# Kernel tuning notes

Measured on AMD Instinct MI355X. Metric: run time of the kernel, lower is better.

Reference implementation:

```python
import jax, jax.numpy as jnp
import numpy as np

B, L, C, NH = 4, 2048, 512, 8
HD = C // NH  # head_dim = 64


def setup_inputs() -> dict:
    key = jax.random.key(0)
    k1, k2, k3, k4 = jax.random.split(key, 4)
    s = 1.0 / np.sqrt(C)
    return {
        "x": jax.random.normal(k1, (B, L, C), dtype=jnp.float32),
        "w_qkv": jax.random.normal(k2, (C, 3 * C), dtype=jnp.float32) * s,
        "b_qkv": jnp.zeros((3 * C,), dtype=jnp.float32),  # zeroed in __init__
        "w_proj": jax.random.normal(k3, (C, C), dtype=jnp.float32) * s,
        "b_proj": jax.random.normal(k4, (C,), dtype=jnp.float32) * 0.01,
    }


def reference(x, w_qkv, b_qkv, w_proj, b_proj):
    Bx, Lx, Cx = x.shape
    qkv = x @ w_qkv + b_qkv                       # [B, L, 3C]
    qkv = qkv.reshape(Bx, Lx, 3, NH, HD)          # 'B L (K H D)'
    qkv = jnp.transpose(qkv, (2, 0, 3, 1, 4))     # 'K B H L D'
    q, k, v = qkv[0], qkv[1], qkv[2]
    scale = 1.0 / np.sqrt(HD)
    scores = jnp.einsum('bhld,bhmd->bhlm', q, k) * scale  # [B, H, L, L]
    attn = jax.nn.softmax(scores, axis=-1)
    out = jnp.einsum('bhlm,bhmd->bhld', attn, v)  # [B, H, L, D]
    out = jnp.transpose(out, (0, 2, 1, 3)).reshape(Bx, Lx, Cx)  # 'B H L D -> B L (H D)'
    return out @ w_proj + b_proj
```

## Files before the change

kernel.cpp:

```cpp
#include <hip/hip_runtime.h>
#include <math.h>

#define B_   4
#define L_   2048
#define C_   512
#define NH_  8
#define HD_  64
#define M_   (B_ * L_)
#define N_QKV 1536

typedef __bf16 bf16x8 __attribute__((ext_vector_type(8)));
typedef float floatx4 __attribute__((ext_vector_type(4)));

__device__ __forceinline__ unsigned pk_bf16(float a, float b) {
  union { float f; unsigned u; } x, y;
  x.f = a; y.f = b;
  unsigned lo = x.u + (0x7fffu + ((x.u >> 16) & 1u));
  unsigned hi = y.u + (0x7fffu + ((y.u >> 16) & 1u));
  return (lo >> 16) | (hi & 0xffff0000u);
}

__device__ __forceinline__ unsigned short bf16_1(float a) {
  union { float f; unsigned u; } x;
  x.f = a;
  return (unsigned short)((x.u + (0x7fffu + ((x.u >> 16) & 1u))) >> 16);
}

__device__ __forceinline__ floatx4 mfma16(bf16x8 a, bf16x8 b, floatx4 c) {
  return __builtin_amdgcn_mfma_f32_16x16x32_bf16(a, b, c, 0, 0, 0);
}

__device__ __forceinline__ void gld_lds16(const void* g, void* s) {
  __builtin_amdgcn_global_load_lds(
      (const __attribute__((address_space(1))) unsigned int*)(g),
      (__attribute__((address_space(3))) unsigned int*)(s), 16, 0, 0);
}

__global__ __launch_bounds__(256) void convert_x_kernel(
    const float* __restrict__ x, unsigned short* __restrict__ xb) {
  size_t i = ((size_t)blockIdx.x * 256 + threadIdx.x) * 8;
  float4 a = *(const float4*)(x + i);
  float4 b = *(const float4*)(x + i + 4);
  uint4 o;
  o.x = pk_bf16(a.x, a.y);
  o.y = pk_bf16(a.z, a.w);
  o.z = pk_bf16(b.x, b.y);
  o.w = pk_bf16(b.z, b.w);
  *(uint4*)(xb + i) = o;
}

__global__ __launch_bounds__(256) void convert_wt_kernel(
    const float* __restrict__ w, unsigned short* __restrict__ wt, int N) {
  __shared__ unsigned short tile[64][68];
  const int t = threadIdx.x;
  const int n0 = blockIdx.x * 64, k0 = blockIdx.y * 64;
  const int r = t >> 4, c4 = (t & 15) * 4;
#pragma unroll
  for (int i = 0; i < 4; ++i) {
    int k = r + i * 16;
    float4 v = *(const float4*)(w + (size_t)(k0 + k) * N + n0 + c4);
    uint2 p;
    p.x = pk_bf16(v.x, v.y);
    p.y = pk_bf16(v.z, v.w);
    *(uint2*)&tile[k][c4] = p;
  }
  __syncthreads();
#pragma unroll
  for (int i = 0; i < 4; ++i) {
    int n = r + i * 16;
    uint2 o;
    o.x = (unsigned)tile[c4 + 0][n] | ((unsigned)tile[c4 + 1][n] << 16);
    o.y = (unsigned)tile[c4 + 2][n] | ((unsigned)tile[c4 + 3][n] << 16);
    *(uint2*)(wt + (size_t)(n0 + n) * 512 + k0 + c4) = o;
  }
}

__global__ __launch_bounds__(256) void qkv_mfma_kernel(
    const unsigned short* __restrict__ A,
    const unsigned short* __restrict__ Bt,
    const float* __restrict__ bias,
    unsigned short* __restrict__ Qd, unsigned short* __restrict__ Kd,
    unsigned short* __restrict__ Vd) {
  __shared__ unsigned short As[4096];
  __shared__ unsigned short Bs[4096];

  const int t = threadIdx.x;
  const int w = t >> 6, l = t & 63;
  const int li = l & 15, lq = l >> 4;
  const int wm = w & 1, wn = w >> 1;
  const int m0 = blockIdx.x * 128;
  const int n0 = blockIdx.y * 128;

  const int inner = (l & 7) ^ (l >> 3);
  const int srow = (l >> 3) * 2 + (inner >> 2);
  const int skb = inner & 3;

  const unsigned short* asrc0 = A + (size_t)(m0 + (2 * w) * 16 + srow) * 512 + skb * 8;
  const unsigned short* asrc1 = A + (size_t)(m0 + (2 * w + 1) * 16 + srow) * 512 + skb * 8;
  const unsigned short* bsrc0 = Bt + (size_t)(n0 + (2 * w) * 16 + srow) * 512 + skb * 8;
  const unsigned short* bsrc1 = Bt + (size_t)(n0 + (2 * w + 1) * 16 + srow) * 512 + skb * 8;
  unsigned short* adst0 = &As[(2 * w) * 512];
  unsigned short* adst1 = &As[(2 * w + 1) * 512];
  unsigned short* bdst0 = &Bs[(2 * w) * 512];
  unsigned short* bdst1 = &Bs[(2 * w + 1) * 512];

  const int foff = (li >> 1) * 128 + ((((li & 1) * 4 + lq)) ^ (li >> 1)) * 16;

  const floatx4 fz = {0.f, 0.f, 0.f, 0.f};
  floatx4 acc[4][4];
#pragma unroll
  for (int i = 0; i < 4; ++i)
#pragma unroll
    for (int j = 0; j < 4; ++j) acc[i][j] = fz;

  for (int kk = 0; kk < 16; ++kk) {
    __syncthreads();
    gld_lds16(asrc0, adst0);
    gld_lds16(asrc1, adst1);
    gld_lds16(bsrc0, bdst0);
    gld_lds16(bsrc1, bdst1);
    asrc0 += 32; asrc1 += 32; bsrc0 += 32; bsrc1 += 32;
    __syncthreads();

    bf16x8 af[4], bf[4];
#pragma unroll
    for (int mt = 0; mt < 4; ++mt)
      af[mt] = *(const bf16x8*)((const char*)As + (wm * 64 + mt * 16) * 64 + foff);
#pragma unroll
    for (int nt = 0; nt < 4; ++nt)
      bf[nt] = *(const bf16x8*)((const char*)Bs + (wn * 64 + nt * 16) * 64 + foff);
#pragma unroll
    for (int mt = 0; mt < 4; ++mt)
#pragma unroll
      for (int nt = 0; nt < 4; ++nt)
        acc[mt][nt] = mfma16(af[mt], bf[nt], acc[mt][nt]);
  }

  const int n0g = n0 + wn * 64;
  const int kk2 = n0g >> 9, h = (n0g >> 6) & 7;
  const int mb = m0 + wm * 64;
  const int b = mb >> 11;
  float bb[4];
#pragma unroll
  for (int nt = 0; nt < 4; ++nt) bb[nt] = bias[n0g + nt * 16 + li];

  if (kk2 < 2) {
    unsigned short* outp = kk2 ? Kd : Qd;
#pragma unroll
    for (int mt = 0; mt < 4; ++mt) {
      int lrow = (mb + mt * 16 + lq * 4) & (L_ - 1);
#pragma unroll
      for (int nt = 0; nt < 4; ++nt) {
        int d = nt * 16 + li;
        unsigned short* p =
            outp + ((size_t)((b * NH_ + h) * L_ + lrow)) * HD_ + d;
#pragma unroll
        for (int r = 0; r < 4; ++r)
          p[(size_t)r * HD_] = bf16_1(acc[mt][nt][r] + bb[nt]);
      }
    }
  } else {
#pragma unroll
    for (int mt = 0; mt < 4; ++mt) {
      int lrow = (mb + mt * 16 + lq * 4) & (L_ - 1);
#pragma unroll
      for (int nt = 0; nt < 4; ++nt) {
        int d = nt * 16 + li;
        uint2 v;
        v.x = pk_bf16(acc[mt][nt][0] + bb[nt], acc[mt][nt][1] + bb[nt]);
        v.y = pk_bf16(acc[mt][nt][2] + bb[nt], acc[mt][nt][3] + bb[nt]);
        *(uint2*)(Vd + ((size_t)((b * NH_ + h) * HD_ + d)) * L_ + lrow) = v;
      }
    }
  }
}

__global__ __launch_bounds__(256) void proj_mfma_kernel(
    const unsigned short* __restrict__ A,
    const unsigned short* __restrict__ Bt,
    const float* __restrict__ bias, float* __restrict__ out) {
  __shared__ unsigned short As[2048];
  __shared__ unsigned short Bs[4096];

  const int t = threadIdx.x;
  const int w = t >> 6, l = t & 63;
  const int li = l & 15, lq = l >> 4;
  const int wm = w & 1, wn = w >> 1;
  const int m0 = blockIdx.x * 64;
  const int n0 = blockIdx.y * 128;

  const int inner = (l & 7) ^ (l >> 3);
  const int srow = (l >> 3) * 2 + (inner >> 2);
  const int skb = inner & 3;

  const unsigned short* asrc0 = A + (size_t)(m0 + w * 16 + srow) * 512 + skb * 8;
  const unsigned short* bsrc0 = Bt + (size_t)(n0 + (2 * w) * 16 + srow) * 512 + skb * 8;
  const unsigned short* bsrc1 = Bt + (size_t)(n0 + (2 * w + 1) * 16 + srow) * 512 + skb * 8;
  unsigned short* adst0 = &As[w * 512];
  unsigned short* bdst0 = &Bs[(2 * w) * 512];
  unsigned short* bdst1 = &Bs[(2 * w + 1) * 512];

  const int foff = (li >> 1) * 128 + ((((li & 1) * 4 + lq)) ^ (li >> 1)) * 16;

  const floatx4 fz = {0.f, 0.f, 0.f, 0.f};
  floatx4 acc[2][4];
#pragma unroll
  for (int i = 0; i < 2; ++i)
#pragma unroll
    for (int j = 0; j < 4; ++j) acc[i][j] = fz;

  for (int kk = 0; kk < 16; ++kk) {
    __syncthreads();
    gld_lds16(asrc0, adst0);
    gld_lds16(bsrc0, bdst0);
    gld_lds16(bsrc1, bdst1);
    asrc0 += 32; bsrc0 += 32; bsrc1 += 32;
    __syncthreads();

    bf16x8 af[2], bf[4];
#pragma unroll
    for (int mt = 0; mt < 2; ++mt)
      af[mt] = *(const bf16x8*)((const char*)As + (wm * 32 + mt * 16) * 64 + foff);
#pragma unroll
    for (int nt = 0; nt < 4; ++nt)
      bf[nt] = *(const bf16x8*)((const char*)Bs + (wn * 64 + nt * 16) * 64 + foff);
#pragma unroll
    for (int mt = 0; mt < 2; ++mt)
#pragma unroll
      for (int nt = 0; nt < 4; ++nt)
        acc[mt][nt] = mfma16(af[mt], bf[nt], acc[mt][nt]);
  }

#pragma unroll
  for (int mt = 0; mt < 2; ++mt) {
    int m = m0 + wm * 32 + mt * 16 + lq * 4;
#pragma unroll
    for (int nt = 0; nt < 4; ++nt) {
      int n = n0 + wn * 64 + nt * 16 + li;
      float bb = bias[n];
#pragma unroll
      for (int r = 0; r < 4; ++r)
        out[(size_t)(m + r) * C_ + n] = acc[mt][nt][r] + bb;
    }
  }
}

__global__ __launch_bounds__(256) void attn_kernel(
    const unsigned short* __restrict__ Qg, const unsigned short* __restrict__ Kg,
    const unsigned short* __restrict__ Vg, unsigned short* __restrict__ AO) {
  __shared__ unsigned short Ks[4096];
  __shared__ unsigned short Vt[4096];
  __shared__ unsigned short Ps[4][32][88];

  const int t  = threadIdx.x;
  const int w  = t >> 6;
  const int l  = t & 63;
  const int li = l & 15;
  const int lq = l >> 4;
  const int bh = blockIdx.y;
  const int m0 = blockIdx.x * 128;

  const unsigned short* ksrc[2];
  const unsigned short* vsrc[2];
  unsigned short* kdst[2];
  unsigned short* vdst[2];
#pragma unroll
  for (int u = 0; u < 2; ++u) {
    int q = 2 * w + u;
    int blk = q * 64 + l;
    int row = blk >> 3, sblk = blk & 7;
    int dblk = sblk ^ ((row >> 2) & 7);
    ksrc[u] = Kg + ((size_t)bh * L_ + row) * HD_ + dblk * 8;
    kdst[u] = &Ks[q * 512];
    int kblk = sblk ^ (row & 7);
    vsrc[u] = Vg + ((size_t)bh * HD_ + row) * L_ + kblk * 8;
    vdst[u] = &Vt[q * 512];
  }

  bf16x8 qf[2][2];
#pragma unroll
  for (int g = 0; g < 2; ++g)
#pragma unroll
    for (int s = 0; s < 2; ++s)
      qf[g][s] = *(const bf16x8*)(Qg +
          ((size_t)bh * L_ + m0 + w * 32 + 16 * g + li) * HD_ + s * 32 + lq * 8);

  const floatx4 fz = {0.f, 0.f, 0.f, 0.f};
  floatx4 O[2][4];
  float lsum[2][4];
#pragma unroll
  for (int g = 0; g < 2; ++g) {
#pragma unroll
    for (int dt = 0; dt < 4; ++dt) O[g][dt] = fz;
#pragma unroll
    for (int r = 0; r < 4; ++r) lsum[g][r] = 0.f;
  }

  const float SC = 0.18033688011f;

  for (int c = 0; c < L_ / 64; ++c) {
    __syncthreads();
#pragma unroll
    for (int u = 0; u < 2; ++u) {
      gld_lds16(ksrc[u], kdst[u]);
      gld_lds16(vsrc[u], vdst[u]);
      ksrc[u] += 64 * HD_;
      vsrc[u] += 64;
    }
    __syncthreads();

    floatx4 sa[2][4];
#pragma unroll
    for (int g = 0; g < 2; ++g)
#pragma unroll
      for (int kt = 0; kt < 4; ++kt) sa[g][kt] = fz;

#pragma unroll
    for (int s = 0; s < 2; ++s) {
#pragma unroll
      for (int kt = 0; kt < 4; ++kt) {
        int key = 4 * li + kt;
        int blk = key * 8 + ((lq + 4 * s) ^ (li & 7));
        bf16x8 kf = *(const bf16x8*)&Ks[blk * 8];
        sa[0][kt] = mfma16(qf[0][s], kf, sa[0][kt]);
        sa[1][kt] = mfma16(qf[1][s], kf, sa[1][kt]);
      }
    }

#pragma unroll
    for (int g = 0; g < 2; ++g) {
      float p[4][4];
#pragma unroll
      for (int kt = 0; kt < 4; ++kt)
#pragma unroll
        for (int r = 0; r < 4; ++r) {
          float pv = __builtin_amdgcn_exp2f(sa[g][kt][r] * SC);
          p[kt][r] = pv;
          lsum[g][r] += pv;
        }
#pragma unroll
      for (int r = 0; r < 4; ++r) {
        uint2 pv;
        pv.x = pk_bf16(p[0][r], p[1][r]);
        pv.y = pk_bf16(p[2][r], p[3][r]);
        *(uint2*)&Ps[w][16 * g + lq * 4 + r][4 * li] = pv;
      }
    }
    __asm__ volatile("" ::: "memory");

#pragma unroll
    for (int s = 0; s < 2; ++s) {
      bf16x8 pa0 = *(const bf16x8*)&Ps[w][li][lq * 8 + 32 * s];
      bf16x8 pa1 = *(const bf16x8*)&Ps[w][16 + li][lq * 8 + 32 * s];
#pragma unroll
      for (int dt = 0; dt < 4; ++dt) {
        int d = 16 * dt + li;
        int blk = d * 8 + ((lq + 4 * s) ^ (li & 7));
        bf16x8 vf = *(const bf16x8*)&Vt[blk * 8];
        O[0][dt] = mfma16(pa0, vf, O[0][dt]);
        O[1][dt] = mfma16(pa1, vf, O[1][dt]);
      }
    }
  }

  const int b = bh >> 3, h = bh & 7;
#pragma unroll
  for (int g = 0; g < 2; ++g) {
    float inv[4];
#pragma unroll
    for (int r = 0; r < 4; ++r) {
      float s = lsum[g][r];
      s += __shfl_xor(s, 1, 64);
      s += __shfl_xor(s, 2, 64);
      s += __shfl_xor(s, 4, 64);
      s += __shfl_xor(s, 8, 64);
      inv[r] = 1.0f / s;
    }
#pragma unroll
    for (int dt = 0; dt < 4; ++dt)
#pragma unroll
      for (int r = 0; r < 4; ++r) {
        int row = m0 + w * 32 + 16 * g + lq * 4 + r;
        AO[((size_t)(b * L_ + row)) * C_ + h * HD_ + 16 * dt + li] =
            bf16_1(O[g][dt][r] * inv[r]);
      }
  }
}

extern "C" void kernel_launch(void* const* d_in, const int* in_sizes, int n_in,
                              void* d_out, int out_size, void* d_ws,
                              size_t ws_size, hipStream_t stream) {
  const float* x      = (const float*)d_in[0];
  const float* w_qkv  = (const float*)d_in[1];
  const float* b_qkv  = (const float*)d_in[2];
  const float* w_proj = (const float*)d_in[3];
  const float* b_proj = (const float*)d_in[4];
  float* out = (float*)d_out;

  unsigned short* ws     = (unsigned short*)d_ws;
  unsigned short* Qd     = ws;
  unsigned short* Kd     = ws + 4194304;
  unsigned short* Vd     = ws + 8388608;
  unsigned short* AO     = ws + 12582912;
  unsigned short* xb     = ws + 16777216;
  unsigned short* wqkvT  = ws + 20971520;
  unsigned short* wprojT = ws + 21757952;

  convert_x_kernel<<<2048, 256, 0, stream>>>(x, xb);
  dim3 gt1(N_QKV / 64, C_ / 64);
  convert_wt_kernel<<<gt1, 256, 0, stream>>>(w_qkv, wqkvT, N_QKV);
  dim3 gt2(C_ / 64, C_ / 64);
  convert_wt_kernel<<<gt2, 256, 0, stream>>>(w_proj, wprojT, C_);

  dim3 g1(M_ / 128, N_QKV / 128);
  qkv_mfma_kernel<<<g1, 256, 0, stream>>>(xb, wqkvT, b_qkv, Qd, Kd, Vd);

  dim3 g2(L_ / 128, B_ * NH_);
  attn_kernel<<<g2, 256, 0, stream>>>(Qd, Kd, Vd, AO);

  dim3 g3(M_ / 64, C_ / 128);
  proj_mfma_kernel<<<g3, 256, 0, stream>>>(AO, wprojT, b_proj, out);
}
```

Baseline: 175.3 us.

## Merge conversions, prescale Q, pre-tile V and keep P in registers in attention

The three conversion kernels become one launch. The softmax scale is folded into Q in the QKV epilogue, and V is written in a pre-tiled layout so attention loads it straight into LDS. The attention kernel computes S transposed (K as the A operand), so the exp'd probabilities are packed in registers and fed directly as the B operand of the PV MFMA, removing the LDS round-trip for P. Row sums shrink to one float per lane and the output is written as packed uint2. The bf16 rounding is simplified to round-half-up via perm, which slightly changes rounding behaviour.

Result: faster. 154.9 us (-11.6%).

```diff
diff --git a/kernel.cpp b/kernel.cpp
--- a/kernel.cpp
+++ b/kernel.cpp
@@ -1,5 +1,4 @@
 #include <hip/hip_runtime.h>
-#include <math.h>
 
 #define B_   4
 #define L_   2048
@@ -11,19 +10,18 @@
 
 typedef __bf16 bf16x8 __attribute__((ext_vector_type(8)));
 typedef float floatx4 __attribute__((ext_vector_type(4)));
-
-__device__ __forceinline__ unsigned pk_bf16(float a, float b) {
+typedef unsigned short ushort_t;
+
+__device__ __forceinline__ unsigned pk2(float a, float b) {
   union { float f; unsigned u; } x, y;
   x.f = a; y.f = b;
-  unsigned lo = x.u + (0x7fffu + ((x.u >> 16) & 1u));
-  unsigned hi = y.u + (0x7fffu + ((y.u >> 16) & 1u));
-  return (lo >> 16) | (hi & 0xffff0000u);
-}
-
-__device__ __forceinline__ unsigned short bf16_1(float a) {
+  return __builtin_amdgcn_perm(y.u + 0x8000u, x.u + 0x8000u, 0x07060302u);
+}
+
+__device__ __forceinline__ ushort_t bf16h(float a) {
   union { float f; unsigned u; } x;
   x.f = a;
-  return (unsigned short)((x.u + (0x7fffu + ((x.u >> 16) & 1u))) >> 16);
+  return (ushort_t)((x.u + 0x8000u) >> 16);
 }
 
 __device__ __forceinline__ floatx4 mfma16(bf16x8 a, bf16x8 b, floatx4 c) {
@@ -36,32 +34,45 @@
       (__attribute__((address_space(3))) unsigned int*)(s), 16, 0, 0);
 }
 
-__global__ __launch_bounds__(256) void convert_x_kernel(
-    const float* __restrict__ x, unsigned short* __restrict__ xb) {
-  size_t i = ((size_t)blockIdx.x * 256 + threadIdx.x) * 8;
-  float4 a = *(const float4*)(x + i);
-  float4 b = *(const float4*)(x + i + 4);
-  uint4 o;
-  o.x = pk_bf16(a.x, a.y);
-  o.y = pk_bf16(a.z, a.w);
-  o.z = pk_bf16(b.x, b.y);
-  o.w = pk_bf16(b.z, b.w);
-  *(uint4*)(xb + i) = o;
-}
-
-__global__ __launch_bounds__(256) void convert_wt_kernel(
-    const float* __restrict__ w, unsigned short* __restrict__ wt, int N) {
-  __shared__ unsigned short tile[64][68];
+__global__ __launch_bounds__(256) void convert_all_kernel(
+    const float* __restrict__ x, const float* __restrict__ wq,
+    const float* __restrict__ wp, ushort_t* __restrict__ xb,
+    ushort_t* __restrict__ wqT, ushort_t* __restrict__ wpT) {
+  __shared__ ushort_t tile[64][68];
   const int t = threadIdx.x;
-  const int n0 = blockIdx.x * 64, k0 = blockIdx.y * 64;
+  const int bid = blockIdx.x;
+  if (bid < 2048) {
+    size_t i = ((size_t)bid * 256 + t) * 8;
+    float4 a = *(const float4*)(x + i);
+    float4 b = *(const float4*)(x + i + 4);
+    uint4 o;
+    o.x = pk2(a.x, a.y);
+    o.y = pk2(a.z, a.w);
+    o.z = pk2(b.x, b.y);
+    o.w = pk2(b.z, b.w);
+    *(uint4*)(xb + i) = o;
+    return;
+  }
+  const float* w;
+  ushort_t* wt;
+  int N, n0, k0;
+  if (bid < 2240) {
+    int b2 = bid - 2048;
+    w = wq; wt = wqT; N = N_QKV;
+    n0 = (b2 % 24) * 64; k0 = (b2 / 24) * 64;
+  } else {
+    int b2 = bid - 2240;
+    w = wp; wt = wpT; N = C_;
+    n0 = (b2 & 7) * 64; k0 = (b2 >> 3) * 64;
+  }
   const int r = t >> 4, c4 = (t & 15) * 4;
 #pragma unroll
   for (int i = 0; i < 4; ++i) {
     int k = r + i * 16;
     float4 v = *(const float4*)(w + (size_t)(k0 + k) * N + n0 + c4);
     uint2 p;
-    p.x = pk_bf16(v.x, v.y);
-    p.y = pk_bf16(v.z, v.w);
+    p.x = pk2(v.x, v.y);
+    p.y = pk2(v.z, v.w);
     *(uint2*)&tile[k][c4] = p;
   }
   __syncthreads();
@@ -76,13 +87,13 @@
 }
 
 __global__ __launch_bounds__(256) void qkv_mfma_kernel(
-    const unsigned short* __restrict__ A,
-    const unsigned short* __restrict__ Bt,
+    const ushort_t* __restrict__ A,
+    const ushort_t* __restrict__ Bt,
     const float* __restrict__ bias,
-    unsigned short* __restrict__ Qd, unsigned short* __restrict__ Kd,
-    unsigned short* __restrict__ Vd) {
-  __shared__ unsigned short As[4096];
-  __shared__ unsigned short Bs[4096];
+    ushort_t* __restrict__ Qd, ushort_t* __restrict__ Kd,
+    ushort_t* __restrict__ Vd) {
+  __shared__ ushort_t As[4096];
+  __shared__ ushort_t Bs[4096];
 
   const int t = threadIdx.x;
   const int w = t >> 6, l = t & 63;
@@ -95,14 +106,14 @@
   const int srow = (l >> 3) * 2 + (inner >> 2);
   const int skb = inner & 3;
 
-  const unsigned short* asrc0 = A + (size_t)(m0 + (2 * w) * 16 + srow) * 512 + skb * 8;
-  const unsigned short* asrc1 = A + (size_t)(m0 + (2 * w + 1) * 16 + srow) * 512 + skb * 8;
-  const unsigned short* bsrc0 = Bt + (size_t)(n0 + (2 * w) * 16 + srow) * 512 + skb * 8;
-  const unsigned short* bsrc1 = Bt + (size_t)(n0 + (2 * w + 1) * 16 + srow) * 512 + skb * 8;
-  unsigned short* adst0 = &As[(2 * w) * 512];
-  unsigned short* adst1 = &As[(2 * w + 1) * 512];
-  unsigned short* bdst0 = &Bs[(2 * w) * 512];
-  unsigned short* bdst1 = &Bs[(2 * w + 1) * 512];
+  const ushort_t* asrc0 = A + (size_t)(m0 + (2 * w) * 16 + srow) * 512 + skb * 8;
+  const ushort_t* asrc1 = A + (size_t)(m0 + (2 * w + 1) * 16 + srow) * 512 + skb * 8;
+  const ushort_t* bsrc0 = Bt + (size_t)(n0 + (2 * w) * 16 + srow) * 512 + skb * 8;
+  const ushort_t* bsrc1 = Bt + (size_t)(n0 + (2 * w + 1) * 16 + srow) * 512 + skb * 8;
+  ushort_t* adst0 = &As[(2 * w) * 512];
+  ushort_t* adst1 = &As[(2 * w + 1) * 512];
+  ushort_t* bdst0 = &Bs[(2 * w) * 512];
+  ushort_t* bdst1 = &Bs[(2 * w + 1) * 512];
 
   const int foff = (li >> 1) * 128 + ((((li & 1) * 4 + lq)) ^ (li >> 1)) * 16;
 
@@ -122,65 +133,210 @@
     asrc0 += 32; asrc1 += 32; bsrc0 += 32; bsrc1 += 32;
     __syncthreads();
 
-    bf16x8 af[4], bf[4];
+    bf16x8 af[4], bfr[4];
 #pragma unroll
     for (int mt = 0; mt < 4; ++mt)
       af[mt] = *(const bf16x8*)((const char*)As + (wm * 64 + mt * 16) * 64 + foff);
 #pragma unroll
     for (int nt = 0; nt < 4; ++nt)
-      bf[nt] = *(const bf16x8*)((const char*)Bs + (wn * 64 + nt * 16) * 64 + foff);
+      bfr[nt] = *(const bf16x8*)((const char*)Bs + (wn * 64 + nt * 16) * 64 + foff);
 #pragma unroll
     for (int mt = 0; mt < 4; ++mt)
 #pragma unroll
       for (int nt = 0; nt < 4; ++nt)
-        acc[mt][nt] = mfma16(af[mt], bf[nt], acc[mt][nt]);
+        acc[mt][nt] = mfma16(af[mt], bfr[nt], acc[mt][nt]);
   }
 
   const int n0g = n0 + wn * 64;
   const int kk2 = n0g >> 9, h = (n0g >> 6) & 7;
   const int mb = m0 + wm * 64;
   const int b = mb >> 11;
+  const int bh = b * NH_ + h;
+  const float SCQ = 0.18033688011f;
   float bb[4];
 #pragma unroll
   for (int nt = 0; nt < 4; ++nt) bb[nt] = bias[n0g + nt * 16 + li];
 
-  if (kk2 < 2) {
-    unsigned short* outp = kk2 ? Kd : Qd;
+  if (kk2 == 0) {
 #pragma unroll
     for (int mt = 0; mt < 4; ++mt) {
       int lrow = (mb + mt * 16 + lq * 4) & (L_ - 1);
 #pragma unroll
       for (int nt = 0; nt < 4; ++nt) {
         int d = nt * 16 + li;
-        unsigned short* p =
-            outp + ((size_t)((b * NH_ + h) * L_ + lrow)) * HD_ + d;
+        ushort_t* p = Qd + ((size_t)bh * L_ + lrow) * HD_ + d;
 #pragma unroll
         for (int r = 0; r < 4; ++r)
-          p[(size_t)r * HD_] = bf16_1(acc[mt][nt][r] + bb[nt]);
-      }
-    }
-  } else {
+          p[(size_t)r * HD_] = bf16h((acc[mt][nt][r] + bb[nt]) * SCQ);
+      }
+    }
+  } else if (kk2 == 1) {
 #pragma unroll
     for (int mt = 0; mt < 4; ++mt) {
       int lrow = (mb + mt * 16 + lq * 4) & (L_ - 1);
 #pragma unroll
       for (int nt = 0; nt < 4; ++nt) {
         int d = nt * 16 + li;
+        ushort_t* p = Kd + ((size_t)bh * L_ + lrow) * HD_ + d;
+#pragma unroll
+        for (int r = 0; r < 4; ++r)
+          p[(size_t)r * HD_] = bf16h(acc[mt][nt][r] + bb[nt]);
+      }
+    }
+  } else {
+#pragma unroll
+    for (int mt = 0; mt < 4; ++mt) {
+      int tb = mb + mt * 16 + lq * 4;
+      int c = (tb >> 6) & 31;
+      int sp = (mt >> 1) & 1;
+      int rem = tb & 31;
+      int lq2 = rem >> 3;
+      int h8 = (rem >> 2) & 1;
+#pragma unroll
+      for (int nt = 0; nt < 4; ++nt) {
+        size_t off = ((size_t)(bh * 32 + c) * 512 +
+                      ((sp * 4 + nt) * 4 + lq2) * 16 + li) * 8 + h8 * 4;
         uint2 v;
-        v.x = pk_bf16(acc[mt][nt][0] + bb[nt], acc[mt][nt][1] + bb[nt]);
-        v.y = pk_bf16(acc[mt][nt][2] + bb[nt], acc[mt][nt][3] + bb[nt]);
-        *(uint2*)(Vd + ((size_t)((b * NH_ + h) * HD_ + d)) * L_ + lrow) = v;
-      }
+        v.x = pk2(acc[mt][nt][0] + bb[nt], acc[mt][nt][1] + bb[nt]);
+        v.y = pk2(acc[mt][nt][2] + bb[nt], acc[mt][nt][3] + bb[nt]);
+        *(uint2*)(Vd + off) = v;
+      }
+    }
+  }
+}
+
+__global__ __launch_bounds__(256) void attn_kernel(
+    const ushort_t* __restrict__ Qg, const ushort_t* __restrict__ Kg,
+    const ushort_t* __restrict__ Vb, ushort_t* __restrict__ AO) {
+  __shared__ ushort_t Ks[4096];
+  __shared__ ushort_t Vs[4096];
+
+  const int t = threadIdx.x;
+  const int w = t >> 6, l = t & 63;
+  const int li = l & 15, lq = l >> 4;
+  const int bh = blockIdx.y;
+  const int m0 = blockIdx.x * 128;
+
+  const ushort_t* ksrc[2];
+  const ushort_t* vsrc[2];
+  ushort_t* kdst[2];
+  ushort_t* vdst[2];
+#pragma unroll
+  for (int u = 0; u < 2; ++u) {
+    int q = 2 * w + u;
+    int p = q * 64 + l;
+    int key = p >> 3, pb = p & 7;
+    int swz = (key & 3) | (((key >> 3) & 1) << 2);
+    ksrc[u] = Kg + ((size_t)bh * L_ + key) * HD_ + (pb ^ swz) * 8;
+    kdst[u] = &Ks[p * 8];
+    vsrc[u] = Vb + ((size_t)bh * 32 * 512 + p) * 8;
+    vdst[u] = &Vs[p * 8];
+  }
+
+  bf16x8 qf[2][2];
+#pragma unroll
+  for (int g = 0; g < 2; ++g)
+#pragma unroll
+    for (int s = 0; s < 2; ++s)
+      qf[g][s] = *(const bf16x8*)(Qg +
+          ((size_t)bh * L_ + m0 + (2 * w + g) * 16 + li) * HD_ + 32 * s + lq * 8);
+
+  const floatx4 fz = {0.f, 0.f, 0.f, 0.f};
+  floatx4 O[2][4];
+  float lsum[2] = {0.f, 0.f};
+#pragma unroll
+  for (int g = 0; g < 2; ++g)
+#pragma unroll
+    for (int dt = 0; dt < 4; ++dt) O[g][dt] = fz;
+
+  const int keybase = 8 * (li >> 2) + (li & 3);
+  const int xsw = li & 7;
+
+  for (int c = 0; c < L_ / 64; ++c) {
+    __syncthreads();
+#pragma unroll
+    for (int u = 0; u < 2; ++u) {
+      gld_lds16(ksrc[u], kdst[u]);
+      gld_lds16(vsrc[u], vdst[u]);
+      ksrc[u] += 64 * HD_;
+      vsrc[u] += 4096;
+    }
+    __syncthreads();
+
+#pragma unroll
+    for (int sp = 0; sp < 2; ++sp) {
+      floatx4 sa[2][2];
+#pragma unroll
+      for (int g = 0; g < 2; ++g)
+#pragma unroll
+        for (int k2 = 0; k2 < 2; ++k2) sa[g][k2] = fz;
+
+#pragma unroll
+      for (int k2 = 0; k2 < 2; ++k2) {
+        const char* rowb = (const char*)Ks + (32 * sp + 4 * k2 + keybase) * 128;
+#pragma unroll
+        for (int s = 0; s < 2; ++s) {
+          bf16x8 kf = *(const bf16x8*)(rowb + ((4 * s + lq) ^ xsw) * 16);
+          sa[0][k2] = mfma16(kf, qf[0][s], sa[0][k2]);
+          sa[1][k2] = mfma16(kf, qf[1][s], sa[1][k2]);
+        }
+      }
+
+      bf16x8 pf[2];
+#pragma unroll
+      for (int g = 0; g < 2; ++g) {
+        float pv[2][4];
+#pragma unroll
+        for (int k2 = 0; k2 < 2; ++k2)
+#pragma unroll
+          for (int r = 0; r < 4; ++r) {
+            float e = __builtin_amdgcn_exp2f(sa[g][k2][r]);
+            pv[k2][r] = e;
+            lsum[g] += e;
+          }
+        uint4 pk;
+        pk.x = pk2(pv[0][0], pv[0][1]);
+        pk.y = pk2(pv[0][2], pv[0][3]);
+        pk.z = pk2(pv[1][0], pv[1][1]);
+        pk.w = pk2(pv[1][2], pv[1][3]);
+        pf[g] = __builtin_bit_cast(bf16x8, pk);
+      }
+
+#pragma unroll
+      for (int dt = 0; dt < 4; ++dt) {
+        bf16x8 vf = *(const bf16x8*)((const char*)Vs +
+            sp * 4096 + dt * 1024 + lq * 256 + li * 16);
+        O[0][dt] = mfma16(vf, pf[0], O[0][dt]);
+        O[1][dt] = mfma16(vf, pf[1], O[1][dt]);
+      }
+    }
+  }
+
+  const int b = bh >> 3, h = bh & 7;
+#pragma unroll
+  for (int g = 0; g < 2; ++g) {
+    float s = lsum[g];
+    s += __shfl_xor(s, 16, 64);
+    s += __shfl_xor(s, 32, 64);
+    float inv = 1.0f / s;
+    int qrow = m0 + (2 * w + g) * 16 + li;
+    ushort_t* base = AO + ((size_t)(b * L_ + qrow)) * C_ + h * HD_ + 4 * lq;
+#pragma unroll
+    for (int dt = 0; dt < 4; ++dt) {
+      uint2 v;
+      v.x = pk2(O[g][dt][0] * inv, O[g][dt][1] * inv);
+      v.y = pk2(O[g][dt][2] * inv, O[g][dt][3] * inv);
+      *(uint2*)(base + 16 * dt) = v;
     }
   }
 }
 
 __global__ __launch_bounds__(256) void proj_mfma_kernel(
-    const unsigned short* __restrict__ A,
-    const unsigned short* __restrict__ Bt,
+    const ushort_t* __restrict__ A,
+    const ushort_t* __restrict__ Bt,
     const float* __restrict__ bias, float* __restrict__ out) {
-  __shared__ unsigned short As[2048];
-  __shared__ unsigned short Bs[4096];
+  __shared__ ushort_t As[2048];
+  __shared__ ushort_t Bs[4096];
 
   const int t = threadIdx.x;
   const int w = t >> 6, l = t & 63;
@@ -193,12 +349,12 @@
   const int srow = (l >> 3) * 2 + (inner >> 2);
   const int skb = inner & 3;
 
-  const unsigned short* asrc0 = A + (size_t)(m0 + w * 16 + srow) * 512 + skb * 8;
-  const unsigned short* bsrc0 = Bt + (size_t)(n0 + (2 * w) * 16 + srow) * 512 + skb * 8;
-  const unsigned short* bsrc1 = Bt + (size_t)(n0 + (2 * w + 1) * 16 + srow) * 512 + skb * 8;
-  unsigned short* adst0 = &As[w * 512];
-  unsigned short* bdst0 = &Bs[(2 * w) * 512];
-  unsigned short* bdst1 = &Bs[(2 * w + 1) * 512];
+  const ushort_t* asrc0 = A + (size_t)(m0 + w * 16 + srow) * 512 + skb * 8;
+  const ushort_t* bsrc0 = Bt + (size_t)(n0 + (2 * w) * 16 + srow) * 512 + skb * 8;
+  const ushort_t* bsrc1 = Bt + (size_t)(n0 + (2 * w + 1) * 16 + srow) * 512 + skb * 8;
+  ushort_t* adst0 = &As[w * 512];
+  ushort_t* bdst0 = &Bs[(2 * w) * 512];
+  ushort_t* bdst1 = &Bs[(2 * w + 1) * 512];
 
   const int foff = (li >> 1) * 128 + ((((li & 1) * 4 + lq)) ^ (li >> 1)) * 16;
 
@@ -217,18 +373,18 @@
     asrc0 += 32; bsrc0 += 32; bsrc1 += 32;
     __syncthreads();
 
-    bf16x8 af[2], bf[4];
+    bf16x8 af[2], bfr[4];
 #pragma unroll
     for (int mt = 0; mt < 2; ++mt)
       af[mt] = *(const bf16x8*)((const char*)As + (wm * 32 + mt * 16) * 64 + foff);
 #pragma unroll
     for (int nt = 0; nt < 4; ++nt)
-      bf[nt] = *(const bf16x8*)((const char*)Bs + (wn * 64 + nt * 16) * 64 + foff);
+      bfr[nt] = *(const bf16x8*)((const char*)Bs + (wn * 64 + nt * 16) * 64 + foff);
 #pragma unroll
     for (int mt = 0; mt < 2; ++mt)
 #pragma unroll
       for (int nt = 0; nt < 4; ++nt)
-        acc[mt][nt] = mfma16(af[mt], bf[nt], acc[mt][nt]);
+        acc[mt][nt] = mfma16(af[mt], bfr[nt], acc[mt][nt]);
   }
 
 #pragma unroll
@@ -242,148 +398,6 @@
       for (int r = 0; r < 4; ++r)
         out[(size_t)(m + r) * C_ + n] = acc[mt][nt][r] + bb;
     }
-  }
-}
-
-__global__ __launch_bounds__(256) void attn_kernel(
-    const unsigned short* __restrict__ Qg, const unsigned short* __restrict__ Kg,
-    const unsigned short* __restrict__ Vg, unsigned short* __restrict__ AO) {
-  __shared__ unsigned short Ks[4096];
-  __shared__ unsigned short Vt[4096];
-  __shared__ unsigned short Ps[4][32][88];
-
-  const int t  = threadIdx.x;
-  const int w  = t >> 6;
-  const int l  = t & 63;
-  const int li = l & 15;
-  const int lq = l >> 4;
-  const int bh = blockIdx.y;
-  const int m0 = blockIdx.x * 128;
-
-  const unsigned short* ksrc[2];
-  const unsigned short* vsrc[2];
-  unsigned short* kdst[2];
-  unsigned short* vdst[2];
-#pragma unroll
-  for (int u = 0; u < 2; ++u) {
-    int q = 2 * w + u;
-    int blk = q * 64 + l;
-    int row = blk >> 3, sblk = blk & 7;
-    int dblk = sblk ^ ((row >> 2) & 7);
-    ksrc[u] = Kg + ((size_t)bh * L_ + row) * HD_ + dblk * 8;
-    kdst[u] = &Ks[q * 512];
-    int kblk = sblk ^ (row & 7);
-    vsrc[u] = Vg + ((size_t)bh * HD_ + row) * L_ + kblk * 8;
-    vdst[u] = &Vt[q * 512];
-  }
-
-  bf16x8 qf[2][2];
-#pragma unroll
-  for (int g = 0; g < 2; ++g)
-#pragma unroll
-    for (int s = 0; s < 2; ++s)
-      qf[g][s] = *(const bf16x8*)(Qg +
-          ((size_t)bh * L_ + m0 + w * 32 + 16 * g + li) * HD_ + s * 32 + lq * 8);
-
-  const floatx4 fz = {0.f, 0.f, 0.f, 0.f};
-  floatx4 O[2][4];
-  float lsum[2][4];
-#pragma unroll
-  for (int g = 0; g < 2; ++g) {
-#pragma unroll
-    for (int dt = 0; dt < 4; ++dt) O[g][dt] = fz;
-#pragma unroll
-    for (int r = 0; r < 4; ++r) lsum[g][r] = 0.f;
-  }
-
-  const float SC = 0.18033688011f;
-
-  for (int c = 0; c < L_ / 64; ++c) {
-    __syncthreads();
-#pragma unroll
-    for (int u = 0; u < 2; ++u) {
-      gld_lds16(ksrc[u], kdst[u]);
-      gld_lds16(vsrc[u], vdst[u]);
-      ksrc[u] += 64 * HD_;
-      vsrc[u] += 64;
-    }
-    __syncthreads();
-
-    floatx4 sa[2][4];
-#pragma unroll
-    for (int g = 0; g < 2; ++g)
-#pragma unroll
-      for (int kt = 0; kt < 4; ++kt) sa[g][kt] = fz;
-
-#pragma unroll
-    for (int s = 0; s < 2; ++s) {
-#pragma unroll
-      for (int kt = 0; kt < 4; ++kt) {
-        int key = 4 * li + kt;
-        int blk = key * 8 + ((lq + 4 * s) ^ (li & 7));
-        bf16x8 kf = *(const bf16x8*)&Ks[blk * 8];
-        sa[0][kt] = mfma16(qf[0][s], kf, sa[0][kt]);
-        sa[1][kt] = mfma16(qf[1][s], kf, sa[1][kt]);
-      }
-    }
-
-#pragma unroll
-    for (int g = 0; g < 2; ++g) {
-      float p[4][4];
-#pragma unroll
-      for (int kt = 0; kt < 4; ++kt)
-#pragma unroll
-        for (int r = 0; r < 4; ++r) {
-          float pv = __builtin_amdgcn_exp2f(sa[g][kt][r] * SC);
-          p[kt][r] = pv;
-          lsum[g][r] += pv;
-        }
-#pragma unroll
-      for (int r = 0; r < 4; ++r) {
-        uint2 pv;
-        pv.x = pk_bf16(p[0][r], p[1][r]);
-        pv.y = pk_bf16(p[2][r], p[3][r]);
-        *(uint2*)&Ps[w][16 * g + lq * 4 + r][4 * li] = pv;
-      }
-    }
-    __asm__ volatile("" ::: "memory");
-
-#pragma unroll
-    for (int s = 0; s < 2; ++s) {
-      bf16x8 pa0 = *(const bf16x8*)&Ps[w][li][lq * 8 + 32 * s];
-      bf16x8 pa1 = *(const bf16x8*)&Ps[w][16 + li][lq * 8 + 32 * s];
-#pragma unroll
-      for (int dt = 0; dt < 4; ++dt) {
-        int d = 16 * dt + li;
-        int blk = d * 8 + ((lq + 4 * s) ^ (li & 7));
-        bf16x8 vf = *(const bf16x8*)&Vt[blk * 8];
-        O[0][dt] = mfma16(pa0, vf, O[0][dt]);
-        O[1][dt] = mfma16(pa1, vf, O[1][dt]);
-      }
-    }
-  }
-
-  const int b = bh >> 3, h = bh & 7;
-#pragma unroll
-  for (int g = 0; g < 2; ++g) {
-    float inv[4];
-#pragma unroll
-    for (int r = 0; r < 4; ++r) {
-      float s = lsum[g][r];
-      s += __shfl_xor(s, 1, 64);
-      s += __shfl_xor(s, 2, 64);
-      s += __shfl_xor(s, 4, 64);
-      s += __shfl_xor(s, 8, 64);
-      inv[r] = 1.0f / s;
-    }
-#pragma unroll
-    for (int dt = 0; dt < 4; ++dt)
-#pragma unroll
-      for (int r = 0; r < 4; ++r) {
-        int row = m0 + w * 32 + 16 * g + lq * 4 + r;
-        AO[((size_t)(b * L_ + row)) * C_ + h * HD_ + 16 * dt + li] =
-            bf16_1(O[g][dt][r] * inv[r]);
-      }
   }
 }
 
@@ -397,20 +411,17 @@
   const float* b_proj = (const float*)d_in[4];
   float* out = (float*)d_out;
 
-  unsigned short* ws     = (unsigned short*)d_ws;
-  unsigned short* Qd     = ws;
-  unsigned short* Kd     = ws + 4194304;
-  unsigned short* Vd     = ws + 8388608;
-  unsigned short* AO     = ws + 12582912;
-  unsigned short* xb     = ws + 16777216;
-  unsigned short* wqkvT  = ws + 20971520;
-  unsigned short* wprojT = ws + 21757952;
-
-  convert_x_kernel<<<2048, 256, 0, stream>>>(x, xb);
-  dim3 gt1(N_QKV / 64, C_ / 64);
-  convert_wt_kernel<<<gt1, 256, 0, stream>>>(w_qkv, wqkvT, N_QKV);
-  dim3 gt2(C_ / 64, C_ / 64);
-  convert_wt_kernel<<<gt2, 256, 0, stream>>>(w_proj, wprojT, C_);
+  ushort_t* ws     = (ushort_t*)d_ws;
+  ushort_t* Qd     = ws;
+  ushort_t* Kd     = ws + 4194304;
+  ushort_t* Vd     = ws + 8388608;
+  ushort_t* AO     = ws + 12582912;
+  ushort_t* xb     = ws + 16777216;
+  ushort_t* wqkvT  = ws + 20971520;
+  ushort_t* wprojT = ws + 21757952;
+
+  convert_all_kernel<<<2304, 256, 0, stream>>>(x, w_qkv, w_proj, xb, wqkvT,
+                                               wprojT);
 
   dim3 g1(M_ / 128, N_QKV / 128);
   qkv_mfma_kernel<<<g1, 256, 0, stream>>>(xb, wqkvT, b_qkv, Qd, Kd, Vd);
```
